# Optimization experiments

Hardware: AMD Instinct MI355X
Metric: run time of the kernel (lower is better)

## Reference

```python
import jax, jax.numpy as jnp
import numpy as np

HID = 128          # hidden_dim
NEV = 16           # n_eigenvectors
CURV = 1.0         # curvature
MAX_NORM = 0.95
N_SCALES = 3


def setup_inputs() -> dict:
    key = jax.random.key(0)
    ks = jax.random.split(key, 12)
    B, N, D = 2048, 128, 64
    A = jax.random.uniform(ks[0], (B, N, N), dtype=jnp.float32)
    A = 0.5 * (A + jnp.swapaxes(A, -1, -2))  # symmetric nonnegative adjacency
    nf = jax.random.normal(ks[1], (B, N, D), dtype=jnp.float32)
    s = 0.05
    return {
        'adjacency': A,
        'node_features': nf,
        'scale_weights': jnp.ones((N_SCALES,), jnp.float32) / N_SCALES,
        'curvature_scale': jnp.array(1.0, jnp.float32),
        'sp_w1': jax.random.normal(ks[2], (NEV, HID), jnp.float32) * s,
        'sp_b1': jnp.zeros((HID,), jnp.float32),
        'sp_w2': jax.random.normal(ks[3], (HID, HID // 2), jnp.float32) * s,
        'sp_b2': jnp.zeros((HID // 2,), jnp.float32),
        'out_w1': jax.random.normal(ks[4], (HID, HID), jnp.float32) * s,
        'out_b1': jnp.zeros((HID,), jnp.float32),
        'out_w2': jax.random.normal(ks[5], (HID, 16), jnp.float32) * s,
        'out_b2': jnp.zeros((16,), jnp.float32),
    }


def reference(adjacency, node_features, scale_weights, curvature_scale,
              sp_w1, sp_b1, sp_w2, sp_b2, out_w1, out_b1, out_w2, out_b2):
    B, N, _ = adjacency.shape
    deg = adjacency.sum(axis=-1)                         # (B, N)
    # normalized Laplacian  L = I - D^{-1/2} A D^{-1/2}
    d_is = (deg + 1e-8) ** -0.5
    sym_adj = adjacency * d_is[:, :, None] * d_is[:, None, :]
    L = jnp.eye(N, dtype=adjacency.dtype) - sym_adj
    evals, evecs = jnp.linalg.eigh(L)                    # ascending, like torch
    k = min(NEV, N - 1)
    sel_vals = evals[:, 1:k + 1]                         # (B, k)  skip trivial eig
    sel_vecs = evecs[:, :, 1:k + 1]                      # (B, N, k)
    # spectral pooling: softmax over -eigenvalues, weighted sum of eigenvectors over nodes
    w = jax.nn.softmax(-sel_vals, axis=-1)               # (B, k)
    pooled = (sel_vecs * w[:, None, :]).sum(axis=1)      # (B, k)
    spectral = jnp.maximum(pooled @ sp_w1 + sp_b1, 0.0) @ sp_w2 + sp_b2  # (B, HID//2)
    # multi-scale diffusion with row-normalized adjacency
    row_adj = adjacency / (deg + 1e-8)[:, :, None]
    ws = jax.nn.softmax(scale_weights)
    feats = node_features
    ms = ws[0] * feats.mean(axis=1)                      # (B, D) with D == HID//2
    for s in range(1, N_SCALES):
        feats = jnp.einsum('bij,bjd->bid', row_adj, feats)
        ms = ms + ws[s] * feats.mean(axis=1)
    combined = jnp.concatenate([spectral, ms], axis=-1)  # (B, HID)
    z_euclidean = jnp.maximum(combined @ out_w1 + out_b1, 0.0) @ out_w2 + out_b2
    # Poincare ball projection (curvature value used as detached scalar, like .item())
    c = CURV * jax.nn.sigmoid(curvature_scale)
    c_const = jax.lax.stop_gradient(c)
    norm = jnp.linalg.norm(z_euclidean, axis=-1, keepdims=True)
    max_r = MAX_NORM / jnp.sqrt(c_const)
    z = z_euclidean * jnp.minimum(1.0, max_r / (norm + 1e-12))
    return z, z_euclidean, spectral, sel_vals, c
```

## Files before the change

### kernel.cpp

```cpp
#include <hip/hip_runtime.h>
#include <math.h>

#define NN 128
#define BLK 256

__device__ __forceinline__ float hsum4(float4 v) { return (v.x + v.y) + (v.z + v.w); }

__device__ __forceinline__ double waveRedD(double v) {
#pragma unroll
  for (int off = 32; off > 0; off >>= 1) v += __shfl_down(v, off, 64);
  return v;
}
__device__ __forceinline__ float waveRedF(float v) {
#pragma unroll
  for (int off = 32; off > 0; off >>= 1) v += __shfl_down(v, off, 64);
  return v;
}
__device__ __forceinline__ float getc(float4 a, int c) {
  return (c == 0) ? a.x : (c == 1) ? a.y : (c == 2) ? a.z : a.w;
}
__device__ __forceinline__ double blockReduceSum(double v, double* red, int tid) {
  v = waveRedD(v);
  __syncthreads();
  if ((tid & 63) == 0) red[tid >> 6] = v;
  __syncthreads();
  return (red[0] + red[1]) + (red[2] + red[3]);
}
__device__ __forceinline__ float startvec(int i, int k) {
  unsigned h = (unsigned)(i * 1664525 + k * 1013904223 + 12345);
  h ^= h >> 13; h *= 2654435761u; h ^= h >> 16;
  return ((float)(h & 0xFFFFFFu) * (1.0f / 16777216.0f)) - 0.5f;
}

extern "C" __global__ void __launch_bounds__(BLK, 4)
holo_kernel(const float* __restrict__ A, const float* __restrict__ F,
            const float* __restrict__ swg, const float* __restrict__ curv,
            const float* __restrict__ W1, const float* __restrict__ Bb1,
            const float* __restrict__ W2, const float* __restrict__ Bb2,
            const float* __restrict__ OW1, const float* __restrict__ OB1,
            const float* __restrict__ OW2, const float* __restrict__ OB2,
            float* __restrict__ out, int B)
{
  __shared__ __align__(16) float wsA[NN * 17];
  __shared__ __align__(16) float wsB[NN * 17];
  __shared__ unsigned swb[16 * 5];
  __shared__ double dd[NN], ee[NN], ee2[NN];
  __shared__ float  tvecf[NN];
  __shared__ double red[4], sc[8];
  __shared__ float  redupf[2], redutf[2], redsigf[2];
  __shared__ double lam[20], blo[17], bhi[17];
  __shared__ int    bcnt[119];
  __shared__ double ssv[16], dred[16];
  __shared__ float  msv[64], pool[16], zrow[16];

  double* dscr  = (double*)wsA;
  float* svec   = wsA + 512;
  float* invdeg = wsA + 640;
  float* gvv    = wsA + 768;
  float* cw     = wsA + 896;
  float* ubuf   = wsA + 1024;
  float* pbuf   = wsA + 1152;
  float* colk   = wsA + 1280;
  float* byv    = wsA;
  float* fscr   = wsB;
  float* sA     = wsB;
  float* comb   = wsB;
  float* hbuf   = wsB + 128;

  const int  tid  = threadIdx.x;
  const int  r    = tid & 127;
  const int  h    = tid >> 7;
  const int  lane = tid & 63;
  const int  wid  = tid >> 6;
  const long b    = blockIdx.x;
  const float* Ab = A + b * (long)(NN * NN);
  const float* Fb = F + b * (long)(NN * 64);

  float4 areg[16];
  {
    const float4* Arow = reinterpret_cast<const float4*>(Ab + (long)r * NN) + 16 * h;
#pragma unroll
    for (int uu = 0; uu < 16; ++uu) areg[uu] = Arow[uu];
  }
  if (tid == 0) {
    const float a0 = swg[0], a1 = swg[1], a2 = swg[2];
    const float mx = fmaxf(a0, fmaxf(a1, a2));
    const float e0 = expf(a0 - mx), e1 = expf(a1 - mx), e2v = expf(a2 - mx);
    const float s = e0 + e1 + e2v;
    sc[0] = (double)(e0 / s); sc[1] = (double)(e1 / s); sc[2] = (double)(e2v / s);
  }
  {
    float4 s4 = make_float4(0.f, 0.f, 0.f, 0.f);
#pragma unroll
    for (int uu = 0; uu < 16; ++uu) {
      s4.x += areg[uu].x; s4.y += areg[uu].y; s4.z += areg[uu].z; s4.w += areg[uu].w;
    }
    dscr[tid] = (double)hsum4(s4);
  }
  __syncthreads();
  if (tid < NN) {
    const double dg = dscr[tid] + dscr[tid + NN] + 1e-8;
    invdeg[tid] = (float)(1.0 / dg);
    svec[tid]   = (float)(1.0 / sqrt(dg));
  }
  __syncthreads();
  {
    const float4* iv4 = (const float4*)invdeg;
    float4 acc = make_float4(0.f, 0.f, 0.f, 0.f);
#pragma unroll
    for (int uu = 0; uu < 16; ++uu) {
      const float4 a = areg[uu], w = iv4[16 * h + uu];
      acc.x = fmaf(a.x, w.x, acc.x); acc.y = fmaf(a.y, w.y, acc.y);
      acc.z = fmaf(a.z, w.z, acc.z); acc.w = fmaf(a.w, w.w, acc.w);
    }
    fscr[tid] = hsum4(acc);
  }
  __syncthreads();
  if (tid < NN) {
    const float gv = fscr[tid] + fscr[tid + NN];
    gvv[tid] = gv;
    ubuf[tid] = gv * invdeg[tid];
  }
  __syncthreads();
  {
    const float4* ub4 = (const float4*)ubuf;
    float4 acc = make_float4(0.f, 0.f, 0.f, 0.f);
#pragma unroll
    for (int uu = 0; uu < 16; ++uu) {
      const float4 a = areg[uu], w = ub4[16 * h + uu];
      acc.x = fmaf(a.x, w.x, acc.x); acc.y = fmaf(a.y, w.y, acc.y);
      acc.z = fmaf(a.z, w.z, acc.z); acc.w = fmaf(a.w, w.w, acc.w);
    }
    fscr[tid] = hsum4(acc);
  }
  __syncthreads();
  if (tid < NN) {
    const float hv = fscr[tid] + fscr[tid + NN];
    cw[tid] = ((float)sc[0] + (float)sc[1] * gvv[tid] + (float)sc[2] * hv) * (1.0f / NN);
  }
  __syncthreads();
  {
    const int d = tid & 63, qt = tid >> 6;
    float acc = 0.0f;
    const float* fb = Fb + qt * 32 * 64;
    for (int n = 0; n < 32; ++n) acc = fmaf(cw[qt * 32 + n], fb[n * 64 + d], acc);
    fscr[tid] = acc;
  }
  __syncthreads();
  if (tid < 64) msv[tid] = (fscr[tid] + fscr[64 + tid]) + (fscr[128 + tid] + fscr[192 + tid]);

  {
    const float sr = svec[r];
    const float4* sv4p = (const float4*)svec;
#pragma unroll
    for (int uu = 0; uu < 16; ++uu) {
      const float4 sv = sv4p[16 * h + uu];
      float4 a = areg[uu];
      a.x = -a.x * sr * sv.x; a.y = -a.y * sr * sv.y;
      a.z = -a.z * sr * sv.z; a.w = -a.w * sr * sv.w;
      areg[uu] = a;
    }
    if ((r >> 6) == h) {
      const int cl = r & 63, du = cl >> 2, dc = cl & 3;
#pragma unroll
      for (int uu = 0; uu < 16; ++uu) if (uu == du) {
        float4 a = areg[uu];
        a.x += (dc == 0) ? 1.f : 0.f; a.y += (dc == 1) ? 1.f : 0.f;
        a.z += (dc == 2) ? 1.f : 0.f; a.w += (dc == 3) ? 1.f : 0.f;
        areg[uu] = a;
      }
    }
  }
  if (tid < NN) tvecf[tid] = 1.0f;
  if (h == 0) {
    const float v0 = areg[0].x;
    colk[r] = v0;
    if (r == 0) dd[0] = (double)v0;
    const float s = waveRedF((r >= 2) ? v0 * v0 : 0.f);
    if (lane == 0) redsigf[wid] = s;
  }
  __syncthreads();

  for (int k = 0; k < NN - 2; ++k) {
    const float sigma  = redsigf[0] + redsigf[1];
    const float alphaf = colk[k + 1];
    double betad; float tauf, sclf;
    if (sigma <= 0.f) { betad = (double)alphaf; tauf = 0.f; sclf = 0.f; }
    else {
      betad = -copysign(sqrt((double)alphaf * (double)alphaf + (double)sigma), (double)alphaf);
      const float betaf = (float)betad;
      tauf = (betaf - alphaf) / betaf;
      sclf = 1.0f / (alphaf - betaf);
    }
    if (tid == 0) ee[k] = betad;
    if (h == 0) ubuf[r] = (r <= k) ? 0.f : (r == k + 1) ? 1.f : colk[r] * sclf;
    __syncthreads();
    {
      float4 acc = make_float4(0.f, 0.f, 0.f, 0.f);
      if (r >= k + 1 && 64 * h + 63 >= k + 1 && tauf != 0.f) {
        const float4* ub4 = (const float4*)ubuf;
#pragma unroll
        for (int uu = 0; uu < 16; ++uu) {
          if (64 * h + 4 * uu + 3 >= k + 1) {
            const float4 a = areg[uu], u4 = ub4[16 * h + uu];
            acc.x = fmaf(a.x, u4.x, acc.x); acc.y = fmaf(a.y, u4.y, acc.y);
            acc.z = fmaf(a.z, u4.z, acc.z); acc.w = fmaf(a.w, u4.w, acc.w);
          }
        }
      }
      fscr[tid] = hsum4(acc);
    }
    __syncthreads();
    if (h == 0) {
      const float p = tauf * (fscr[r] + fscr[r + NN]);
      pbuf[r] = p;
      const float uv = ubuf[r];
      const float s1 = waveRedF(uv * p);
      const float s2 = waveRedF(uv * tvecf[r]);
      if (lane == 0) { redupf[wid] = s1; redutf[wid] = s2; }
    }
    __syncthreads();
    {
      const float K   = 0.5f * tauf * (redupf[0] + redupf[1]);
      const float tut = tauf * (redutf[0] + redutf[1]);
      if (r >= k + 1) {
        const float ur = ubuf[r];
        const float qr = fmaf(-K, ur, pbuf[r]);
        if (64 * h + 63 >= k + 1) {
          const float4* ub4 = (const float4*)ubuf;
          const float4* pb4 = (const float4*)pbuf;
#pragma unroll
          for (int uu = 0; uu < 16; ++uu) {
            if (64 * h + 4 * uu + 3 >= k + 1) {
              const float4 u4 = ub4[16 * h + uu], p4 = pb4[16 * h + uu];
              float4 a = areg[uu];
              const float qx = fmaf(-K, u4.x, p4.x);
              const float qy = fmaf(-K, u4.y, p4.y);
              const float qz = fmaf(-K, u4.z, p4.z);
              const float qw = fmaf(-K, u4.w, p4.w);
              a.x -= ur * qx + qr * u4.x;
              a.y -= ur * qy + qr * u4.y;
              a.z -= ur * qz + qr * u4.z;
              a.w -= ur * qw + qr * u4.w;
              areg[uu] = a;
            }
          }
        }
        if (h == 0) tvecf[r] -= tut * ubuf[r];
      }
      const int hstar = (k + 1) >> 6;
      if (h == hstar) {
        float sigp = 0.0f;
        if (r >= k + 1) {
          const int cl = (k + 1) - 64 * hstar, du = cl >> 2, dc = cl & 3;
          float val = 0.f;
#pragma unroll
          for (int uu = 0; uu < 16; ++uu) if (uu == du) val = getc(areg[uu], dc);
          if (r == k + 1) dd[k + 1] = (double)val;
          else {
            colk[r] = val;
            if (r >= k + 3) sigp = val * val;
          }
        }
        const float s = waveRedF(sigp);
        if (lane == 0) redsigf[wid & 1] = s;
      }
    }
    __syncthreads();
  }
  if (tid == 0)       ee[NN - 2] = (double)colk[NN - 1];
  if (tid == BLK - 1) dd[NN - 1] = (double)areg[15].w;
  __syncthreads();

  if (tid < NN - 1) ee2[tid] = ee[tid] * ee[tid];
  if (tid == 0) {
    double lo = 1e300, hi = -1e300;
    for (int i = 0; i < NN; ++i) {
      const double rr = ((i > 0) ? fabs(ee[i - 1]) : 0.0) + ((i < NN - 1) ? fabs(ee[i]) : 0.0);
      lo = fmin(lo, dd[i] - rr);
      hi = fmax(hi, dd[i] + rr);
    }
    sc[4] = lo - 1e-6; sc[5] = hi + 1e-6;
  }
  __syncthreads();
  if (tid < 17) { blo[tid] = sc[4]; bhi[tid] = sc[5]; }
  __syncthreads();
  for (int round = 0; round < 11; ++round) {
    if (tid < 119) {
      const int ke = tid / 7, j = tid % 7;
      const double lo = blo[ke], hi = bhi[ke];
      const double x = lo + (hi - lo) * ((double)(j + 1) * 0.125);
      int cnt = 0;
      double pm = 1.0, p = dd[0] - x;
      if (p < 0.0) cnt++;
      for (int i = 1; i < NN; ++i) {
        const double pn = (dd[i] - x) * p - ee2[i - 1] * pm;
        pm = p; p = pn;
        if ((p < 0.0) != (pm < 0.0)) cnt++;
        const double ap = fabs(p);
        if (ap > 1e100)                   { p *= 1e-100; pm *= 1e-100; }
        else if (ap < 1e-100 && ap > 0.0) { p *= 1e100;  pm *= 1e100; }
      }
      bcnt[tid] = cnt;
    }
    __syncthreads();
    if (tid < 17) {
      const double lo = blo[tid], hi = bhi[tid];
      const double w8 = (hi - lo) * 0.125;
      double nlo = lo, nhi = hi;
      for (int jj = 0; jj < 7; ++jj) {
        const double x = lo + w8 * (double)(jj + 1);
        if (bcnt[tid * 7 + jj] <= tid) nlo = x; else { nhi = x; break; }
      }
      blo[tid] = nlo; bhi[tid] = nhi;
    }
    __syncthreads();
  }
  if (tid < 17) lam[tid] = 0.5 * (blo[tid] + bhi[tid]);
  __syncthreads();

  if (tid < 16) {
    const double lk = lam[tid + 1];
    for (int it = 0; it < 2; ++it) {
      float beta = (float)(dd[0] - lk);
      float gam  = (float)ee[0];
      float rr   = (it == 0) ? startvec(0, tid) : byv[0 * 17 + tid];
      unsigned bw = 0;
      for (int i = 1; i < NN; ++i) {
        const int j = i - 1;
        const float ai = (float)ee[i - 1];
        const float bi = (float)(dd[i] - lk);
        const float ci = (i < NN - 1) ? (float)ee[i] : 0.0f;
        const float ri = (it == 0) ? startvec(i, tid) : byv[i * 17 + tid];
        if (fabsf(beta) >= fabsf(ai)) {
          float piv = (beta == 0.0f) ? 1e-25f : beta;
          const float mm = ai / piv;
          sA [j * 17 + tid] = piv;
          byv[j * 17 + tid] = rr;
          beta = bi - mm * gam;  gam = ci;  rr = ri - mm * rr;
        } else {
          const float mm = beta / ai;
          sA [j * 17 + tid] = mm;
          byv[j * 17 + tid] = ri;
          beta = gam - mm * bi;  gam = -mm * ci;  rr = rr - mm * ri;
          bw |= 1u << (j & 31);
        }
        if ((j & 31) == 31) { swb[tid * 5 + (j >> 5)] = bw; bw = 0; }
      }
      if (beta == 0.0f) beta = 1e-25f;
      sA [127 * 17 + tid] = beta;
      byv[127 * 17 + tid] = rr;
      swb[tid * 5 + 3] = bw;
      float y1 = 0.0f, y2 = 0.0f;
      for (int j = NN - 1; j >= 0; --j) {
        const bool sj = (swb[tid * 5 + (j >> 5)] >> (j & 31)) & 1;
        const bool sjm1 = (j > 0) ? ((swb[tid * 5 + ((j - 1) >> 5)] >> ((j - 1) & 31)) & 1) : false;
        float u0, u1, u2;
        if (sj) {
          u0 = (float)ee[j];
          u1 = (float)(dd[j + 1] - lk);
          u2 = (j < NN - 2) ? (float)ee[j + 1] : 0.0f;
        } else {
          u0 = sA[j * 17 + tid];
          const float ej = (j < NN - 1) ? (float)ee[j] : 0.0f;
          u1 = sjm1 ? (-sA[(j - 1) * 17 + tid] * ej) : ej;
          u2 = 0.0f;
        }
        const float yy = (byv[j * 17 + tid] - u1 * y1 - u2 * y2) / u0;
        byv[j * 17 + tid] = yy;
        y2 = y1; y1 = yy;
      }
      double nrm = 0.0;
      for (int i = 0; i < NN; ++i) { const double v = (double)byv[i * 17 + tid]; nrm += v * v; }
      const double inv = 1.0 / sqrt(nrm);
      for (int i = 0; i < NN; ++i) byv[i * 17 + tid] = (float)((double)byv[i * 17 + tid] * inv);
    }
  }
  __syncthreads();

  for (int kk = 1; kk < 16; ++kk) {
    const int j = tid >> 3, s8 = tid & 7;
    double part = 0.0;
    if (j < kk)
      for (int i = s8 * 16; i < s8 * 16 + 16; ++i)
        part += (double)byv[i * 17 + j] * (double)byv[i * 17 + kk];
    for (int off = 4; off > 0; off >>= 1) part += __shfl_down(part, off, 8);
    __syncthreads();
    if (s8 == 0 && j < kk) dred[j] = part;
    __syncthreads();
    if (tid < NN) {
      double acc = (double)byv[tid * 17 + kk];
      for (int j2 = 0; j2 < kk; ++j2) acc -= dred[j2] * (double)byv[tid * 17 + j2];
      byv[tid * 17 + kk] = (float)acc;
    }
    __syncthreads();
    double p2 = 0.0;
    if (tid < NN) { const double v = (double)byv[tid * 17 + kk]; p2 = v * v; }
    const double n2 = blockReduceSum(p2, red, tid);
    if (tid < NN) byv[tid * 17 + kk] = (float)((double)byv[tid * 17 + kk] / sqrt(n2));
    __syncthreads();
  }

  if (tid < NN) {
    const int j = tid >> 3, s8 = tid & 7;
    double part = 0.0;
    for (int i = s8 * 16; i < s8 * 16 + 16; ++i)
      part += (double)tvecf[i] * (double)byv[i * 17 + j];
    for (int off = 4; off > 0; off >>= 1) part += __shfl_down(part, off, 8);
    if (s8 == 0) ssv[j] = part;
  }
  __syncthreads();
  if (tid == 0) {
    float lv[16], ev[16];
    float mx = -1e30f;
    for (int i = 0; i < 16; ++i) { lv[i] = (float)lam[i + 1]; mx = fmaxf(mx, -lv[i]); }
    float se = 0.0f;
    for (int i = 0; i < 16; ++i) { ev[i] = expf(-lv[i] - mx); se += ev[i]; }
    for (int i = 0; i < 16; ++i) pool[i] = (ev[i] / se) * (float)ssv[i];
  }
  __syncthreads();

  if (tid < NN) {
    float acc = Bb1[tid];
    for (int i = 0; i < 16; ++i) acc = fmaf(pool[i], W1[i * 128 + tid], acc);
    hbuf[tid] = fmaxf(acc, 0.0f);
  }
  __syncthreads();
  if (tid < 64) {
    float acc = Bb2[tid];
    for (int i = 0; i < 128; ++i) acc = fmaf(hbuf[i], W2[i * 64 + tid], acc);
    comb[tid] = acc;
  } else if (tid < NN) {
    comb[tid] = msv[tid - 64];
  }
  __syncthreads();
  if (tid < NN) {
    float acc = OB1[tid];
    for (int i = 0; i < 128; ++i) acc = fmaf(comb[i], OW1[i * 128 + tid], acc);
    hbuf[tid] = fmaxf(acc, 0.0f);
  }
  __syncthreads();
  if (tid < 16) {
    float acc = OB2[tid];
    for (int i = 0; i < 128; ++i) acc = fmaf(hbuf[i], OW2[i * 16 + tid], acc);
    zrow[tid] = acc;
  }
  __syncthreads();

  const long zeoff = (long)B * 16;
  const long spoff = (long)B * 32;
  const long svoff = (long)B * 32 + (long)B * 64;
  const long coff  = svoff + (long)B * 16;

  if (tid == 0) {
    const float c = 1.0f / (1.0f + expf(-curv[0]));
    float nrm = 0.0f;
    for (int i = 0; i < 16; ++i) nrm += zrow[i] * zrow[i];
    nrm = sqrtf(nrm);
    const float max_r = 0.95f / sqrtf(c);
    sc[3] = (double)fminf(1.0f, max_r / (nrm + 1e-12f));
    if (b == 0) out[coff] = c;
  }
  __syncthreads();
  if (tid < 16) {
    const float fac = (float)sc[3];
    out[b * 16 + tid]          = zrow[tid] * fac;
    out[zeoff + b * 16 + tid]  = zrow[tid];
    out[svoff + b * 16 + tid]  = (float)lam[tid + 1];
  }
  if (tid < 64) out[spoff + b * 64 + tid] = comb[tid];
}

extern "C" void kernel_launch(void* const* d_in, const int* in_sizes, int n_in,
                              void* d_out, int out_size, void* d_ws, size_t ws_size,
                              hipStream_t stream) {
  const float* A    = (const float*)d_in[0];
  const float* F    = (const float*)d_in[1];
  const float* swg  = (const float*)d_in[2];
  const float* curv = (const float*)d_in[3];
  const float* W1   = (const float*)d_in[4];
  const float* Bb1  = (const float*)d_in[5];
  const float* W2   = (const float*)d_in[6];
  const float* Bb2  = (const float*)d_in[7];
  const float* OW1  = (const float*)d_in[8];
  const float* OB1  = (const float*)d_in[9];
  const float* OW2  = (const float*)d_in[10];
  const float* OB2  = (const float*)d_in[11];
  float* out = (float*)d_out;
  const int B = in_sizes[0] / (128 * 128);

  holo_kernel<<<dim3(B), dim3(BLK), 0, stream>>>(
      A, F, swg, curv, W1, Bb1, W2, Bb2, OW1, OB1, OW2, OB2, out, B);
}
```

Measured before the change: 1.493 ms.

## Pack two graphs per 512-thread block and drop per-column guards in Householder loop

Each block now processes two batch elements, 256 threads each, with duplicated shared-memory arrays and the grid halved. The per-float4 column guards inside the tridiagonalization rank-update loops are removed, so every unrolled iteration runs unconditionally. The likely aim is to fit more concurrent work per CU given the __launch_bounds__(BLK,4) setting and to cut branch overhead. The cost is that the two halves of a block share every __syncthreads, shared memory per block doubles, and register pressure under the 512-thread launch bound may force spills of the 64-float areg array.

```diff
diff --git a/kernel.cpp b/kernel.cpp
--- a/kernel.cpp
+++ b/kernel.cpp
@@ -2,7 +2,8 @@
 #include <math.h>
 
 #define NN 128
-#define BLK 256
+#define BLK 512
+#define WSF (NN * 17)
 
 __device__ __forceinline__ float hsum4(float4 v) { return (v.x + v.y) + (v.z + v.w); }
 
@@ -19,12 +20,12 @@
 __device__ __forceinline__ float getc(float4 a, int c) {
   return (c == 0) ? a.x : (c == 1) ? a.y : (c == 2) ? a.z : a.w;
 }
-__device__ __forceinline__ double blockReduceSum(double v, double* red, int tid) {
+__device__ __forceinline__ double blockReduceSumM(double v, double* red4, int t) {
   v = waveRedD(v);
   __syncthreads();
-  if ((tid & 63) == 0) red[tid >> 6] = v;
-  __syncthreads();
-  return (red[0] + red[1]) + (red[2] + red[3]);
+  if ((t & 63) == 0) red4[t >> 6] = v;
+  __syncthreads();
+  return (red4[0] + red4[1]) + (red4[2] + red4[3]);
 }
 __device__ __forceinline__ float startvec(int i, int k) {
   unsigned h = (unsigned)(i * 1664525 + k * 1013904223 + 12345);
@@ -41,40 +42,66 @@
             const float* __restrict__ OW2, const float* __restrict__ OB2,
             float* __restrict__ out, int B)
 {
-  __shared__ __align__(16) float wsA[NN * 17];
-  __shared__ __align__(16) float wsB[NN * 17];
-  __shared__ unsigned swb[16 * 5];
-  __shared__ double dd[NN], ee[NN], ee2[NN];
-  __shared__ float  tvecf[NN];
-  __shared__ double red[4], sc[8];
-  __shared__ float  redupf[2], redutf[2], redsigf[2];
-  __shared__ double lam[20], blo[17], bhi[17];
-  __shared__ int    bcnt[119];
-  __shared__ double ssv[16], dred[16];
-  __shared__ float  msv[64], pool[16], zrow[16];
-
-  double* dscr  = (double*)wsA;
-  float* svec   = wsA + 512;
-  float* invdeg = wsA + 640;
-  float* gvv    = wsA + 768;
-  float* cw     = wsA + 896;
-  float* ubuf   = wsA + 1024;
-  float* pbuf   = wsA + 1152;
-  float* colk   = wsA + 1280;
-  float* byv    = wsA;
-  float* fscr   = wsB;
-  float* sA     = wsB;
-  float* comb   = wsB;
-  float* hbuf   = wsB + 128;
-
-  const int  tid  = threadIdx.x;
-  const int  r    = tid & 127;
-  const int  h    = tid >> 7;
-  const int  lane = tid & 63;
-  const int  wid  = tid >> 6;
-  const long b    = blockIdx.x;
-  const float* Ab = A + b * (long)(NN * NN);
-  const float* Fb = F + b * (long)(NN * 64);
+  __shared__ __align__(16) float wsA[2 * WSF];
+  __shared__ __align__(16) float wsB[2 * WSF];
+  __shared__ unsigned swb_s[2 * 80];
+  __shared__ double dd_s[2 * NN], ee_s[2 * NN], ee2_s[2 * NN];
+  __shared__ float  tvecf_s[2 * NN];
+  __shared__ double red_s[2 * 4], sc_s[2 * 8];
+  __shared__ float  redupf_s[2 * 2], redutf_s[2 * 2], redsigf_s[2 * 2];
+  __shared__ double lam_s[2 * 20], blo_s[2 * 17], bhi_s[2 * 17];
+  __shared__ int    bcnt_s[2 * 119];
+  __shared__ double ssv_s[2 * 16], dred_s[2 * 16];
+  __shared__ float  msv_s[2 * 64], pool_s[2 * 16], zrow_s[2 * 16];
+
+  const int  tid = threadIdx.x;
+  const int  mid = tid >> 8;
+  const int  t   = tid & 255;
+  const int  r   = t & 127;
+  const int  h   = t >> 7;
+  const int  lane = t & 63;
+  const int  widm = t >> 6;
+
+  float*  wsAm = wsA + mid * WSF;
+  float*  wsBm = wsB + mid * WSF;
+  unsigned* swb = swb_s + mid * 80;
+  double* dd  = dd_s  + mid * NN;
+  double* ee  = ee_s  + mid * NN;
+  double* ee2 = ee2_s + mid * NN;
+  float*  tvecf = tvecf_s + mid * NN;
+  double* red = red_s + mid * 4;
+  double* sc  = sc_s  + mid * 8;
+  float*  redupf  = redupf_s  + mid * 2;
+  float*  redutf  = redutf_s  + mid * 2;
+  float*  redsigf = redsigf_s + mid * 2;
+  double* lam = lam_s + mid * 20;
+  double* blo = blo_s + mid * 17;
+  double* bhi = bhi_s + mid * 17;
+  int*    bcnt = bcnt_s + mid * 119;
+  double* ssv  = ssv_s  + mid * 16;
+  double* dred = dred_s + mid * 16;
+  float*  msv  = msv_s  + mid * 64;
+  float*  pool = pool_s + mid * 16;
+  float*  zrow = zrow_s + mid * 16;
+
+  double* dscr  = (double*)wsAm;
+  float* svec   = wsAm + 512;
+  float* invdeg = wsAm + 640;
+  float* gvv    = wsAm + 768;
+  float* cw     = wsAm + 896;
+  float* ubuf   = wsAm + 1024;
+  float* pbuf   = wsAm + 1152;
+  float* colk   = wsAm + 1280;
+  float* byv    = wsAm;
+  float* fscr   = wsBm;
+  float* sA     = wsBm;
+  float* comb   = wsBm;
+  float* hbuf   = wsBm + 128;
+
+  const long bm = 2L * blockIdx.x + mid;
+  const long bc = (bm < B) ? bm : (long)(B - 1);
+  const float* Ab = A + bc * (long)(NN * NN);
+  const float* Fb = F + bc * (long)(NN * 64);
 
   float4 areg[16];
   {
@@ -82,7 +109,7 @@
 #pragma unroll
     for (int uu = 0; uu < 16; ++uu) areg[uu] = Arow[uu];
   }
-  if (tid == 0) {
+  if (t == 0) {
     const float a0 = swg[0], a1 = swg[1], a2 = swg[2];
     const float mx = fmaxf(a0, fmaxf(a1, a2));
     const float e0 = expf(a0 - mx), e1 = expf(a1 - mx), e2v = expf(a2 - mx);
@@ -95,13 +122,13 @@
     for (int uu = 0; uu < 16; ++uu) {
       s4.x += areg[uu].x; s4.y += areg[uu].y; s4.z += areg[uu].z; s4.w += areg[uu].w;
     }
-    dscr[tid] = (double)hsum4(s4);
-  }
-  __syncthreads();
-  if (tid < NN) {
-    const double dg = dscr[tid] + dscr[tid + NN] + 1e-8;
-    invdeg[tid] = (float)(1.0 / dg);
-    svec[tid]   = (float)(1.0 / sqrt(dg));
+    dscr[t] = (double)hsum4(s4);
+  }
+  __syncthreads();
+  if (t < NN) {
+    const double dg = dscr[t] + dscr[t + NN] + 1e-8;
+    invdeg[t] = (float)(1.0 / dg);
+    svec[t]   = (float)(1.0 / sqrt(dg));
   }
   __syncthreads();
   {
@@ -113,13 +140,13 @@
       acc.x = fmaf(a.x, w.x, acc.x); acc.y = fmaf(a.y, w.y, acc.y);
       acc.z = fmaf(a.z, w.z, acc.z); acc.w = fmaf(a.w, w.w, acc.w);
     }
-    fscr[tid] = hsum4(acc);
-  }
-  __syncthreads();
-  if (tid < NN) {
-    const float gv = fscr[tid] + fscr[tid + NN];
-    gvv[tid] = gv;
-    ubuf[tid] = gv * invdeg[tid];
+    fscr[t] = hsum4(acc);
+  }
+  __syncthreads();
+  if (t < NN) {
+    const float gv = fscr[t] + fscr[t + NN];
+    gvv[t] = gv;
+    ubuf[t] = gv * invdeg[t];
   }
   __syncthreads();
   {
@@ -131,23 +158,23 @@
       acc.x = fmaf(a.x, w.x, acc.x); acc.y = fmaf(a.y, w.y, acc.y);
       acc.z = fmaf(a.z, w.z, acc.z); acc.w = fmaf(a.w, w.w, acc.w);
     }
-    fscr[tid] = hsum4(acc);
-  }
-  __syncthreads();
-  if (tid < NN) {
-    const float hv = fscr[tid] + fscr[tid + NN];
-    cw[tid] = ((float)sc[0] + (float)sc[1] * gvv[tid] + (float)sc[2] * hv) * (1.0f / NN);
+    fscr[t] = hsum4(acc);
+  }
+  __syncthreads();
+  if (t < NN) {
+    const float hv = fscr[t] + fscr[t + NN];
+    cw[t] = ((float)sc[0] + (float)sc[1] * gvv[t] + (float)sc[2] * hv) * (1.0f / NN);
   }
   __syncthreads();
   {
-    const int d = tid & 63, qt = tid >> 6;
+    const int d = t & 63, qt = t >> 6;
     float acc = 0.0f;
     const float* fb = Fb + qt * 32 * 64;
     for (int n = 0; n < 32; ++n) acc = fmaf(cw[qt * 32 + n], fb[n * 64 + d], acc);
-    fscr[tid] = acc;
-  }
-  __syncthreads();
-  if (tid < 64) msv[tid] = (fscr[tid] + fscr[64 + tid]) + (fscr[128 + tid] + fscr[192 + tid]);
+    fscr[t] = acc;
+  }
+  __syncthreads();
+  if (t < 64) msv[t] = (fscr[t] + fscr[64 + t]) + (fscr[128 + t] + fscr[192 + t]);
 
   {
     const float sr = svec[r];
@@ -171,13 +198,13 @@
       }
     }
   }
-  if (tid < NN) tvecf[tid] = 1.0f;
+  if (t < NN) tvecf[t] = 1.0f;
   if (h == 0) {
     const float v0 = areg[0].x;
     colk[r] = v0;
     if (r == 0) dd[0] = (double)v0;
     const float s = waveRedF((r >= 2) ? v0 * v0 : 0.f);
-    if (lane == 0) redsigf[wid] = s;
+    if (lane == 0) redsigf[widm] = s;
   }
   __syncthreads();
 
@@ -192,7 +219,7 @@
       tauf = (betaf - alphaf) / betaf;
       sclf = 1.0f / (alphaf - betaf);
     }
-    if (tid == 0) ee[k] = betad;
+    if (t == 0) ee[k] = betad;
     if (h == 0) ubuf[r] = (r <= k) ? 0.f : (r == k + 1) ? 1.f : colk[r] * sclf;
     __syncthreads();
     {
@@ -201,14 +228,12 @@
         const float4* ub4 = (const float4*)ubuf;
 #pragma unroll
         for (int uu = 0; uu < 16; ++uu) {
-          if (64 * h + 4 * uu + 3 >= k + 1) {
-            const float4 a = areg[uu], u4 = ub4[16 * h + uu];
-            acc.x = fmaf(a.x, u4.x, acc.x); acc.y = fmaf(a.y, u4.y, acc.y);
-            acc.z = fmaf(a.z, u4.z, acc.z); acc.w = fmaf(a.w, u4.w, acc.w);
-          }
+          const float4 a = areg[uu], u4 = ub4[16 * h + uu];
+          acc.x = fmaf(a.x, u4.x, acc.x); acc.y = fmaf(a.y, u4.y, acc.y);
+          acc.z = fmaf(a.z, u4.z, acc.z); acc.w = fmaf(a.w, u4.w, acc.w);
         }
       }
-      fscr[tid] = hsum4(acc);
+      fscr[t] = hsum4(acc);
     }
     __syncthreads();
     if (h == 0) {
@@ -217,7 +242,7 @@
       const float uv = ubuf[r];
       const float s1 = waveRedF(uv * p);
       const float s2 = waveRedF(uv * tvecf[r]);
-      if (lane == 0) { redupf[wid] = s1; redutf[wid] = s2; }
+      if (lane == 0) { redupf[widm] = s1; redutf[widm] = s2; }
     }
     __syncthreads();
     {
@@ -231,19 +256,17 @@
           const float4* pb4 = (const float4*)pbuf;
 #pragma unroll
           for (int uu = 0; uu < 16; ++uu) {
-            if (64 * h + 4 * uu + 3 >= k + 1) {
-              const float4 u4 = ub4[16 * h + uu], p4 = pb4[16 * h + uu];
-              float4 a = areg[uu];
-              const float qx = fmaf(-K, u4.x, p4.x);
-              const float qy = fmaf(-K, u4.y, p4.y);
-              const float qz = fmaf(-K, u4.z, p4.z);
-              const float qw = fmaf(-K, u4.w, p4.w);
-              a.x -= ur * qx + qr * u4.x;
-              a.y -= ur * qy + qr * u4.y;
-              a.z -= ur * qz + qr * u4.z;
-              a.w -= ur * qw + qr * u4.w;
-              areg[uu] = a;
-            }
+            const float4 u4 = ub4[16 * h + uu], p4 = pb4[16 * h + uu];
+            float4 a = areg[uu];
+            const float qx = fmaf(-K, u4.x, p4.x);
+            const float qy = fmaf(-K, u4.y, p4.y);
+            const float qz = fmaf(-K, u4.z, p4.z);
+            const float qw = fmaf(-K, u4.w, p4.w);
+            a.x -= ur * qx + qr * u4.x;
+            a.y -= ur * qy + qr * u4.y;
+            a.z -= ur * qz + qr * u4.z;
+            a.w -= ur * qw + qr * u4.w;
+            areg[uu] = a;
           }
         }
         if (h == 0) tvecf[r] -= tut * ubuf[r];
@@ -263,17 +286,17 @@
           }
         }
         const float s = waveRedF(sigp);
-        if (lane == 0) redsigf[wid & 1] = s;
-      }
-    }
-    __syncthreads();
-  }
-  if (tid == 0)       ee[NN - 2] = (double)colk[NN - 1];
-  if (tid == BLK - 1) dd[NN - 1] = (double)areg[15].w;
-  __syncthreads();
-
-  if (tid < NN - 1) ee2[tid] = ee[tid] * ee[tid];
-  if (tid == 0) {
+        if (lane == 0) redsigf[widm & 1] = s;
+      }
+    }
+    __syncthreads();
+  }
+  if (t == 0)   ee[NN - 2] = (double)colk[NN - 1];
+  if (t == 255) dd[NN - 1] = (double)areg[15].w;
+  __syncthreads();
+
+  if (t < NN - 1) ee2[t] = ee[t] * ee[t];
+  if (t == 0) {
     double lo = 1e300, hi = -1e300;
     for (int i = 0; i < NN; ++i) {
       const double rr = ((i > 0) ? fabs(ee[i - 1]) : 0.0) + ((i < NN - 1) ? fabs(ee[i]) : 0.0);
@@ -283,11 +306,11 @@
     sc[4] = lo - 1e-6; sc[5] = hi + 1e-6;
   }
   __syncthreads();
-  if (tid < 17) { blo[tid] = sc[4]; bhi[tid] = sc[5]; }
+  if (t < 17) { blo[t] = sc[4]; bhi[t] = sc[5]; }
   __syncthreads();
   for (int round = 0; round < 11; ++round) {
-    if (tid < 119) {
-      const int ke = tid / 7, j = tid % 7;
+    if (t < 119) {
+      const int ke = t / 7, j = t % 7;
       const double lo = blo[ke], hi = bhi[ke];
       const double x = lo + (hi - lo) * ((double)(j + 1) * 0.125);
       int cnt = 0;
@@ -301,85 +324,85 @@
         if (ap > 1e100)                   { p *= 1e-100; pm *= 1e-100; }
         else if (ap < 1e-100 && ap > 0.0) { p *= 1e100;  pm *= 1e100; }
       }
-      bcnt[tid] = cnt;
-    }
-    __syncthreads();
-    if (tid < 17) {
-      const double lo = blo[tid], hi = bhi[tid];
+      bcnt[t] = cnt;
+    }
+    __syncthreads();
+    if (t < 17) {
+      const double lo = blo[t], hi = bhi[t];
       const double w8 = (hi - lo) * 0.125;
       double nlo = lo, nhi = hi;
       for (int jj = 0; jj < 7; ++jj) {
         const double x = lo + w8 * (double)(jj + 1);
-        if (bcnt[tid * 7 + jj] <= tid) nlo = x; else { nhi = x; break; }
-      }
-      blo[tid] = nlo; bhi[tid] = nhi;
-    }
-    __syncthreads();
-  }
-  if (tid < 17) lam[tid] = 0.5 * (blo[tid] + bhi[tid]);
-  __syncthreads();
-
-  if (tid < 16) {
-    const double lk = lam[tid + 1];
+        if (bcnt[t * 7 + jj] <= t) nlo = x; else { nhi = x; break; }
+      }
+      blo[t] = nlo; bhi[t] = nhi;
+    }
+    __syncthreads();
+  }
+  if (t < 17) lam[t] = 0.5 * (blo[t] + bhi[t]);
+  __syncthreads();
+
+  if (t < 16) {
+    const double lk = lam[t + 1];
     for (int it = 0; it < 2; ++it) {
       float beta = (float)(dd[0] - lk);
       float gam  = (float)ee[0];
-      float rr   = (it == 0) ? startvec(0, tid) : byv[0 * 17 + tid];
+      float rr   = (it == 0) ? startvec(0, t) : byv[0 * 17 + t];
       unsigned bw = 0;
       for (int i = 1; i < NN; ++i) {
         const int j = i - 1;
         const float ai = (float)ee[i - 1];
         const float bi = (float)(dd[i] - lk);
         const float ci = (i < NN - 1) ? (float)ee[i] : 0.0f;
-        const float ri = (it == 0) ? startvec(i, tid) : byv[i * 17 + tid];
+        const float ri = (it == 0) ? startvec(i, t) : byv[i * 17 + t];
         if (fabsf(beta) >= fabsf(ai)) {
           float piv = (beta == 0.0f) ? 1e-25f : beta;
           const float mm = ai / piv;
-          sA [j * 17 + tid] = piv;
-          byv[j * 17 + tid] = rr;
+          sA [j * 17 + t] = piv;
+          byv[j * 17 + t] = rr;
           beta = bi - mm * gam;  gam = ci;  rr = ri - mm * rr;
         } else {
           const float mm = beta / ai;
-          sA [j * 17 + tid] = mm;
-          byv[j * 17 + tid] = ri;
+          sA [j * 17 + t] = mm;
+          byv[j * 17 + t] = ri;
           beta = gam - mm * bi;  gam = -mm * ci;  rr = rr - mm * ri;
           bw |= 1u << (j & 31);
         }
-        if ((j & 31) == 31) { swb[tid * 5 + (j >> 5)] = bw; bw = 0; }
+        if ((j & 31) == 31) { swb[t * 5 + (j >> 5)] = bw; bw = 0; }
       }
       if (beta == 0.0f) beta = 1e-25f;
-      sA [127 * 17 + tid] = beta;
-      byv[127 * 17 + tid] = rr;
-      swb[tid * 5 + 3] = bw;
+      sA [127 * 17 + t] = beta;
+      byv[127 * 17 + t] = rr;
+      swb[t * 5 + 3] = bw;
       float y1 = 0.0f, y2 = 0.0f;
       for (int j = NN - 1; j >= 0; --j) {
-        const bool sj = (swb[tid * 5 + (j >> 5)] >> (j & 31)) & 1;
-        const bool sjm1 = (j > 0) ? ((swb[tid * 5 + ((j - 1) >> 5)] >> ((j - 1) & 31)) & 1) : false;
+        const bool sj = (swb[t * 5 + (j >> 5)] >> (j & 31)) & 1;
+        const bool sjm1 = (j > 0) ? ((swb[t * 5 + ((j - 1) >> 5)] >> ((j - 1) & 31)) & 1) : false;
         float u0, u1, u2;
         if (sj) {
           u0 = (float)ee[j];
           u1 = (float)(dd[j + 1] - lk);
           u2 = (j < NN - 2) ? (float)ee[j + 1] : 0.0f;
         } else {
-          u0 = sA[j * 17 + tid];
+          u0 = sA[j * 17 + t];
           const float ej = (j < NN - 1) ? (float)ee[j] : 0.0f;
-          u1 = sjm1 ? (-sA[(j - 1) * 17 + tid] * ej) : ej;
+          u1 = sjm1 ? (-sA[(j - 1) * 17 + t] * ej) : ej;
           u2 = 0.0f;
         }
-        const float yy = (byv[j * 17 + tid] - u1 * y1 - u2 * y2) / u0;
-        byv[j * 17 + tid] = yy;
+        const float yy = (byv[j * 17 + t] - u1 * y1 - u2 * y2) / u0;
+        byv[j * 17 + t] = yy;
         y2 = y1; y1 = yy;
       }
       double nrm = 0.0;
-      for (int i = 0; i < NN; ++i) { const double v = (double)byv[i * 17 + tid]; nrm += v * v; }
+      for (int i = 0; i < NN; ++i) { const double v = (double)byv[i * 17 + t]; nrm += v * v; }
       const double inv = 1.0 / sqrt(nrm);
-      for (int i = 0; i < NN; ++i) byv[i * 17 + tid] = (float)((double)byv[i * 17 + tid] * inv);
+      for (int i = 0; i < NN; ++i) byv[i * 17 + t] = (float)((double)byv[i * 17 + t] * inv);
     }
   }
   __syncthreads();
 
   for (int kk = 1; kk < 16; ++kk) {
-    const int j = tid >> 3, s8 = tid & 7;
+    const int j = t >> 3, s8 = t & 7;
     double part = 0.0;
     if (j < kk)
       for (int i = s8 * 16; i < s8 * 16 + 16; ++i)
@@ -388,21 +411,21 @@
     __syncthreads();
     if (s8 == 0 && j < kk) dred[j] = part;
     __syncthreads();
-    if (tid < NN) {
-      double acc = (double)byv[tid * 17 + kk];
-      for (int j2 = 0; j2 < kk; ++j2) acc -= dred[j2] * (double)byv[tid * 17 + j2];
-      byv[tid * 17 + kk] = (float)acc;
+    if (t < NN) {
+      double acc = (double)byv[t * 17 + kk];
+      for (int j2 = 0; j2 < kk; ++j2) acc -= dred[j2] * (double)byv[t * 17 + j2];
+      byv[t * 17 + kk] = (float)acc;
     }
     __syncthreads();
     double p2 = 0.0;
-    if (tid < NN) { const double v = (double)byv[tid * 17 + kk]; p2 = v * v; }
-    const double n2 = blockReduceSum(p2, red, tid);
-    if (tid < NN) byv[tid * 17 + kk] = (float)((double)byv[tid * 17 + kk] / sqrt(n2));
-    __syncthreads();
-  }
-
-  if (tid < NN) {
-    const int j = tid >> 3, s8 = tid & 7;
+    if (t < NN) { const double v = (double)byv[t * 17 + kk]; p2 = v * v; }
+    const double n2 = blockReduceSumM(p2, red, t);
+    if (t < NN) byv[t * 17 + kk] = (float)((double)byv[t * 17 + kk] / sqrt(n2));
+    __syncthreads();
+  }
+
+  if (t < NN) {
+    const int j = t >> 3, s8 = t & 7;
     double part = 0.0;
     for (int i = s8 * 16; i < s8 * 16 + 16; ++i)
       part += (double)tvecf[i] * (double)byv[i * 17 + j];
@@ -410,7 +433,7 @@
     if (s8 == 0) ssv[j] = part;
   }
   __syncthreads();
-  if (tid == 0) {
+  if (t == 0) {
     float lv[16], ev[16];
     float mx = -1e30f;
     for (int i = 0; i < 16; ++i) { lv[i] = (float)lam[i + 1]; mx = fmaxf(mx, -lv[i]); }
@@ -420,30 +443,30 @@
   }
   __syncthreads();
 
-  if (tid < NN) {
-    float acc = Bb1[tid];
-    for (int i = 0; i < 16; ++i) acc = fmaf(pool[i], W1[i * 128 + tid], acc);
-    hbuf[tid] = fmaxf(acc, 0.0f);
-  }
-  __syncthreads();
-  if (tid < 64) {
-    float acc = Bb2[tid];
-    for (int i = 0; i < 128; ++i) acc = fmaf(hbuf[i], W2[i * 64 + tid], acc);
-    comb[tid] = acc;
-  } else if (tid < NN) {
-    comb[tid] = msv[tid - 64];
-  }
-  __syncthreads();
-  if (tid < NN) {
-    float acc = OB1[tid];
-    for (int i = 0; i < 128; ++i) acc = fmaf(comb[i], OW1[i * 128 + tid], acc);
-    hbuf[tid] = fmaxf(acc, 0.0f);
-  }
-  __syncthreads();
-  if (tid < 16) {
-    float acc = OB2[tid];
-    for (int i = 0; i < 128; ++i) acc = fmaf(hbuf[i], OW2[i * 16 + tid], acc);
-    zrow[tid] = acc;
+  if (t < NN) {
+    float acc = Bb1[t];
+    for (int i = 0; i < 16; ++i) acc = fmaf(pool[i], W1[i * 128 + t], acc);
+    hbuf[t] = fmaxf(acc, 0.0f);
+  }
+  __syncthreads();
+  if (t < 64) {
+    float acc = Bb2[t];
+    for (int i = 0; i < 128; ++i) acc = fmaf(hbuf[i], W2[i * 64 + t], acc);
+    comb[t] = acc;
+  } else if (t < NN) {
+    comb[t] = msv[t - 64];
+  }
+  __syncthreads();
+  if (t < NN) {
+    float acc = OB1[t];
+    for (int i = 0; i < 128; ++i) acc = fmaf(comb[i], OW1[i * 128 + t], acc);
+    hbuf[t] = fmaxf(acc, 0.0f);
+  }
+  __syncthreads();
+  if (t < 16) {
+    float acc = OB2[t];
+    for (int i = 0; i < 128; ++i) acc = fmaf(hbuf[i], OW2[i * 16 + t], acc);
+    zrow[t] = acc;
   }
   __syncthreads();
 
@@ -452,23 +475,25 @@
   const long svoff = (long)B * 32 + (long)B * 64;
   const long coff  = svoff + (long)B * 16;
 
-  if (tid == 0) {
+  if (t == 0) {
     const float c = 1.0f / (1.0f + expf(-curv[0]));
     float nrm = 0.0f;
     for (int i = 0; i < 16; ++i) nrm += zrow[i] * zrow[i];
     nrm = sqrtf(nrm);
     const float max_r = 0.95f / sqrtf(c);
     sc[3] = (double)fminf(1.0f, max_r / (nrm + 1e-12f));
-    if (b == 0) out[coff] = c;
-  }
-  __syncthreads();
-  if (tid < 16) {
-    const float fac = (float)sc[3];
-    out[b * 16 + tid]          = zrow[tid] * fac;
-    out[zeoff + b * 16 + tid]  = zrow[tid];
-    out[svoff + b * 16 + tid]  = (float)lam[tid + 1];
-  }
-  if (tid < 64) out[spoff + b * 64 + tid] = comb[tid];
+    if (bm == 0) out[coff] = c;
+  }
+  __syncthreads();
+  if (bm < B) {
+    if (t < 16) {
+      const float fac = (float)sc[3];
+      out[bm * 16 + t]          = zrow[t] * fac;
+      out[zeoff + bm * 16 + t]  = zrow[t];
+      out[svoff + bm * 16 + t]  = (float)lam[t + 1];
+    }
+    if (t < 64) out[spoff + bm * 64 + t] = comb[t];
+  }
 }
 
 extern "C" void kernel_launch(void* const* d_in, const int* in_sizes, int n_in,
@@ -489,6 +514,6 @@
   float* out = (float*)d_out;
   const int B = in_sizes[0] / (128 * 128);
 
-  holo_kernel<<<dim3(B), dim3(BLK), 0, stream>>>(
+  holo_kernel<<<dim3((B + 1) / 2), dim3(BLK), 0, stream>>>(
       A, F, swg, curv, W1, Bb1, W2, Bb2, OW1, OB1, OW2, OB2, out, B);
 }
```

Measured after the change: 1.678 ms. 12.4% more time.

## Remove a barrier per Householder step by using raw column and lookahead buffer

Applied to the files above, without the earlier changes.

The tridiagonalization loop no longer builds the Householder vector u in shared memory before the matrix-vector product. It multiplies A by the raw column x and corrects with a scale and the next column, which is prefetched one step ahead into a double buffer. This drops one __syncthreads per iteration and coarsens the per-float4 guards into groups of four. The launch bounds drop from 4 to 3 blocks per SM, which allows more registers but may lower occupancy. The rescaled algebra can also change float rounding.

```diff
diff --git a/kernel.cpp b/kernel.cpp
--- a/kernel.cpp
+++ b/kernel.cpp
@@ -32,7 +32,7 @@
   return ((float)(h & 0xFFFFFFu) * (1.0f / 16777216.0f)) - 0.5f;
 }
 
-extern "C" __global__ void __launch_bounds__(BLK, 4)
+extern "C" __global__ void __launch_bounds__(BLK, 3)
 holo_kernel(const float* __restrict__ A, const float* __restrict__ F,
             const float* __restrict__ swg, const float* __restrict__ curv,
             const float* __restrict__ W1, const float* __restrict__ Bb1,
@@ -61,6 +61,7 @@
   float* ubuf   = wsA + 1024;
   float* pbuf   = wsA + 1152;
   float* colk   = wsA + 1280;
+  float* wbuf2  = wsA + 1408;
   float* byv    = wsA;
   float* fscr   = wsB;
   float* sA     = wsB;
@@ -71,7 +72,7 @@
   const int  r    = tid & 127;
   const int  h    = tid >> 7;
   const int  lane = tid & 63;
-  const int  wid  = tid >> 6;
+  const int  widm = tid >> 6;
   const long b    = blockIdx.x;
   const float* Ab = A + b * (long)(NN * NN);
   const float* Fb = F + b * (long)(NN * 64);
@@ -173,15 +174,19 @@
   }
   if (tid < NN) tvecf[tid] = 1.0f;
   if (h == 0) {
-    const float v0 = areg[0].x;
-    colk[r] = v0;
-    if (r == 0) dd[0] = (double)v0;
-    const float s = waveRedF((r >= 2) ? v0 * v0 : 0.f);
-    if (lane == 0) redsigf[wid] = s;
+    const float c0 = areg[0].x;
+    const float c1 = areg[0].y;
+    colk[r]  = (r >= 1) ? c0 : 0.f;
+    wbuf2[r] = (r >= 1) ? c1 : 0.f;
+    if (r == 0) dd[0] = (double)c0;
+    const float s = waveRedF((r >= 2) ? c0 * c0 : 0.f);
+    if (lane == 0) redsigf[widm] = s;
   }
   __syncthreads();
 
   for (int k = 0; k < NN - 2; ++k) {
+    const float* wc = wbuf2 + (k & 1) * NN;
+    float*       wn = wbuf2 + ((k + 1) & 1) * NN;
     const float sigma  = redsigf[0] + redsigf[1];
     const float alphaf = colk[k + 1];
     double betad; float tauf, sclf;
@@ -193,18 +198,19 @@
       sclf = 1.0f / (alphaf - betaf);
     }
     if (tid == 0) ee[k] = betad;
-    if (h == 0) ubuf[r] = (r <= k) ? 0.f : (r == k + 1) ? 1.f : colk[r] * sclf;
-    __syncthreads();
     {
+      const float4* xk4 = (const float4*)colk;
       float4 acc = make_float4(0.f, 0.f, 0.f, 0.f);
-      if (r >= k + 1 && 64 * h + 63 >= k + 1 && tauf != 0.f) {
-        const float4* ub4 = (const float4*)ubuf;
-#pragma unroll
-        for (int uu = 0; uu < 16; ++uu) {
-          if (64 * h + 4 * uu + 3 >= k + 1) {
-            const float4 a = areg[uu], u4 = ub4[16 * h + uu];
-            acc.x = fmaf(a.x, u4.x, acc.x); acc.y = fmaf(a.y, u4.y, acc.y);
-            acc.z = fmaf(a.z, u4.z, acc.z); acc.w = fmaf(a.w, u4.w, acc.w);
+      if (r >= k + 1) {
+#pragma unroll
+        for (int g = 0; g < 4; ++g) {
+          if (64 * h + 16 * g + 15 >= k + 1) {
+#pragma unroll
+            for (int uu = 4 * g; uu < 4 * g + 4; ++uu) {
+              const float4 a = areg[uu], x4 = xk4[16 * h + uu];
+              acc.x = fmaf(a.x, x4.x, acc.x); acc.y = fmaf(a.y, x4.y, acc.y);
+              acc.z = fmaf(a.z, x4.z, acc.z); acc.w = fmaf(a.w, x4.w, acc.w);
+            }
           }
         }
       }
@@ -212,26 +218,43 @@
     }
     __syncthreads();
     if (h == 0) {
-      const float p = tauf * (fscr[r] + fscr[r + NN]);
-      pbuf[r] = p;
-      const float uv = ubuf[r];
-      const float s1 = waveRedF(uv * p);
-      const float s2 = waveRedF(uv * tvecf[r]);
-      if (lane == 0) { redupf[wid] = s1; redutf[wid] = s2; }
+      const float xr = colk[r];
+      const float wr = wc[r];
+      const float ur = (r <= k) ? 0.f : (r == k + 1) ? 1.f : sclf * xr;
+      const float pr = (r <= k) ? 0.f
+                     : tauf * (sclf * (fscr[r] + fscr[r + NN]) + (1.f - sclf * alphaf) * wr);
+      ubuf[r] = ur; pbuf[r] = pr;
+      const float s1 = waveRedF(ur * pr);
+      const float s2 = waveRedF(ur * tvecf[r]);
+      if (lane == 0) { redupf[widm] = s1; redutf[widm] = s2; }
     }
     __syncthreads();
     {
       const float K   = 0.5f * tauf * (redupf[0] + redupf[1]);
       const float tut = tauf * (redutf[0] + redutf[1]);
+      if (h == 0) {
+        const float qk1 = pbuf[k + 1] - K;
+        const float ur0 = ubuf[r];
+        const float qr0 = fmaf(-K, ur0, pbuf[r]);
+        tvecf[r] -= tut * ur0;
+        float cn = 0.f;
+        if (r >= k + 2)      { cn = wc[r] - ur0 * qk1 - qr0; colk[r] = cn; }
+        else if (r == k + 1) colk[r] = 0.f;
+        const float sp = (r >= k + 3) ? cn * cn : 0.f;
+        const float s = waveRedF(sp);
+        if (lane == 0) redsigf[widm] = s;
+        if (r == 0) dd[k + 1] = (double)(wc[k + 1] - 2.f * qk1);
+      }
       if (r >= k + 1) {
         const float ur = ubuf[r];
         const float qr = fmaf(-K, ur, pbuf[r]);
-        if (64 * h + 63 >= k + 1) {
-          const float4* ub4 = (const float4*)ubuf;
-          const float4* pb4 = (const float4*)pbuf;
-#pragma unroll
-          for (int uu = 0; uu < 16; ++uu) {
-            if (64 * h + 4 * uu + 3 >= k + 1) {
+        const float4* ub4 = (const float4*)ubuf;
+        const float4* pb4 = (const float4*)pbuf;
+#pragma unroll
+        for (int g = 0; g < 4; ++g) {
+          if (64 * h + 16 * g + 15 >= k + 1) {
+#pragma unroll
+            for (int uu = 4 * g; uu < 4 * g + 4; ++uu) {
               const float4 u4 = ub4[16 * h + uu], p4 = pb4[16 * h + uu];
               float4 a = areg[uu];
               const float qx = fmaf(-K, u4.x, p4.x);
@@ -246,24 +269,14 @@
             }
           }
         }
-        if (h == 0) tvecf[r] -= tut * ubuf[r];
-      }
-      const int hstar = (k + 1) >> 6;
-      if (h == hstar) {
-        float sigp = 0.0f;
-        if (r >= k + 1) {
-          const int cl = (k + 1) - 64 * hstar, du = cl >> 2, dc = cl & 3;
-          float val = 0.f;
-#pragma unroll
-          for (int uu = 0; uu < 16; ++uu) if (uu == du) val = getc(areg[uu], dc);
-          if (r == k + 1) dd[k + 1] = (double)val;
-          else {
-            colk[r] = val;
-            if (r >= k + 3) sigp = val * val;
-          }
-        }
-        const float s = waveRedF(sigp);
-        if (lane == 0) redsigf[wid & 1] = s;
+      }
+      const int hstar2 = (k + 2) >> 6;
+      if (h == hstar2 && r >= k + 2) {
+        const int cl = (k + 2) - 64 * hstar2, du = cl >> 2, dc = cl & 3;
+        float val = 0.f;
+#pragma unroll
+        for (int uu = 0; uu < 16; ++uu) if (uu == du) val = getc(areg[uu], dc);
+        wn[r] = val;
       }
     }
     __syncthreads();
```

After: 1.854 ms. 1.24x slower.

## Finish last Householder tridiagonalization steps in a single wavefront without block barriers

Applied to the files above, without the earlier changes.

The Householder tridiagonalization loop now stops at step 95. The remaining 32x32 trailing submatrix is copied to shared memory and reduced by one wavefront, using register-resident rows, readlane broadcasts and xor-shuffle reductions. This removes three block-wide __syncthreads per step for the last 31 steps, where most threads had little work. The trade-off is that sigma and beta are now computed in float instead of double, so accuracy may differ slightly.

```diff
diff --git a/kernel.cpp b/kernel.cpp
--- a/kernel.cpp
+++ b/kernel.cpp
@@ -6,6 +6,10 @@
 
 __device__ __forceinline__ float hsum4(float4 v) { return (v.x + v.y) + (v.z + v.w); }
 
+__device__ __forceinline__ float bcast(float v, int lane) {
+  return __int_as_float(__builtin_amdgcn_readlane(__float_as_int(v), lane));
+}
+
 __device__ __forceinline__ double waveRedD(double v) {
 #pragma unroll
   for (int off = 32; off > 0; off >>= 1) v += __shfl_down(v, off, 64);
@@ -14,6 +18,11 @@
 __device__ __forceinline__ float waveRedF(float v) {
 #pragma unroll
   for (int off = 32; off > 0; off >>= 1) v += __shfl_down(v, off, 64);
+  return v;
+}
+__device__ __forceinline__ float waveAllRedF(float v) {
+#pragma unroll
+  for (int off = 32; off > 0; off >>= 1) v += __shfl_xor(v, off, 64);
   return v;
 }
 __device__ __forceinline__ float getc(float4 a, int c) {
@@ -63,6 +72,7 @@
   float* colk   = wsA + 1280;
   float* byv    = wsA;
   float* fscr   = wsB;
+  float* cornr  = wsB + 256;
   float* sA     = wsB;
   float* comb   = wsB;
   float* hbuf   = wsB + 128;
@@ -71,7 +81,7 @@
   const int  r    = tid & 127;
   const int  h    = tid >> 7;
   const int  lane = tid & 63;
-  const int  wid  = tid >> 6;
+  const int  widm = tid >> 6;
   const long b    = blockIdx.x;
   const float* Ab = A + b * (long)(NN * NN);
   const float* Fb = F + b * (long)(NN * 64);
@@ -177,11 +187,11 @@
     colk[r] = v0;
     if (r == 0) dd[0] = (double)v0;
     const float s = waveRedF((r >= 2) ? v0 * v0 : 0.f);
-    if (lane == 0) redsigf[wid] = s;
-  }
-  __syncthreads();
-
-  for (int k = 0; k < NN - 2; ++k) {
+    if (lane == 0) redsigf[widm] = s;
+  }
+  __syncthreads();
+
+  for (int k = 0; k < 95; ++k) {
     const float sigma  = redsigf[0] + redsigf[1];
     const float alphaf = colk[k + 1];
     double betad; float tauf, sclf;
@@ -217,7 +227,7 @@
       const float uv = ubuf[r];
       const float s1 = waveRedF(uv * p);
       const float s2 = waveRedF(uv * tvecf[r]);
-      if (lane == 0) { redupf[wid] = s1; redutf[wid] = s2; }
+      if (lane == 0) { redupf[widm] = s1; redutf[widm] = s2; }
     }
     __syncthreads();
     {
@@ -263,13 +273,74 @@
           }
         }
         const float s = waveRedF(sigp);
-        if (lane == 0) redsigf[wid & 1] = s;
-      }
-    }
-    __syncthreads();
-  }
-  if (tid == 0)       ee[NN - 2] = (double)colk[NN - 1];
-  if (tid == BLK - 1) dd[NN - 1] = (double)areg[15].w;
+        if (lane == 0) redsigf[widm & 1] = s;
+      }
+    }
+    __syncthreads();
+  }
+
+  if (h == 1 && r >= 96) {
+    const int rl = r - 96;
+#pragma unroll
+    for (int uu = 8; uu < 16; ++uu) {
+      const int j0 = (uu - 8) * 4;
+      cornr[rl * 33 + j0 + 0] = areg[uu].x;
+      cornr[rl * 33 + j0 + 1] = areg[uu].y;
+      cornr[rl * 33 + j0 + 2] = areg[uu].z;
+      cornr[rl * 33 + j0 + 3] = areg[uu].w;
+    }
+  }
+  __syncthreads();
+
+  if (tid < 64) {
+    const bool own = (lane < 32);
+    float arow[32];
+#pragma unroll
+    for (int j = 0; j < 32; ++j) arow[j] = own ? cornr[lane * 33 + j] : 0.f;
+    float colval = own ? colk[96 + lane] : 0.f;
+    float tv     = own ? tvecf[96 + lane] : 0.f;
+
+    for (int k = 95; k <= 125; ++k) {
+      const int kk = k - 95;
+      const float sigp  = (lane >= kk + 1 && lane < 32) ? colval * colval : 0.f;
+      const float sigma = waveAllRedF(sigp);
+      const float alphaf = bcast(colval, kk);
+      float betaf, tauf, sclf;
+      if (sigma <= 0.f) { betaf = alphaf; tauf = 0.f; sclf = 0.f; }
+      else {
+        betaf = -copysignf(sqrtf(fmaf(alphaf, alphaf, sigma)), alphaf);
+        tauf = (betaf - alphaf) / betaf;
+        sclf = 1.0f / (alphaf - betaf);
+      }
+      if (lane == 0) ee[k] = (double)betaf;
+      const bool live = own && (lane >= kk);
+      const float u_me = !live ? 0.f : (lane == kk ? 1.f : colval * sclf);
+      float y = 0.f;
+#pragma unroll
+      for (int j = 0; j < 32; ++j) y = fmaf(arow[j], bcast(u_me, j), y);
+      const float p_me = live ? tauf * y : 0.f;
+      const float up = waveAllRedF(u_me * p_me);
+      const float ut = waveAllRedF(u_me * tv);
+      const float K   = 0.5f * tauf * up;
+      const float tut = tauf * ut;
+      const float q_me = fmaf(-K, u_me, p_me);
+      tv -= tut * u_me;
+      float ncol = 0.f;
+#pragma unroll
+      for (int j = 0; j < 32; ++j) {
+        const float uj = bcast(u_me, j);
+        const float qj = bcast(q_me, j);
+        arow[j] -= u_me * qj + q_me * uj;
+        if (j == kk) ncol = arow[j];
+      }
+      if (lane == 0) dd[k + 1] = (double)bcast(ncol, kk);
+      colval = (lane > kk && lane < 32) ? ncol : 0.f;
+    }
+    const float e126 = bcast(colval, 31);
+    const float d127 = bcast(arow[31], 31);
+    if (lane == 0) { ee[NN - 2] = (double)e126; dd[NN - 1] = (double)d127; }
+    if (own) tvecf[96 + lane] = tv;
+  }
   __syncthreads();
 
   if (tid < NN - 1) ee2[tid] = ee[tid] * ee[tid];
```

New measurement: 1.442 ms. -3.4%, faster.
